# Kernel optimization log

Measured on AMD Instinct MI355X. Metric: run time of the kernel, lower is better.

Reference implementation:

```python
import jax, jax.numpy as jnp
import numpy as np

ECNUM = 100
CA1NUM = 100
CA3NUM = 100
ACTNUM = 2
TRACKLEN = 100
SIGMA = 5.0
BS = 4096


def setup_inputs() -> dict:
    key = jax.random.key(0)
    ks = jax.random.split(key, 10)
    cue_train = jax.random.randint(ks[0], (BS, TRACKLEN), 0, 3).astype(jnp.int32) - 1  # values in {-1,0,1}
    ec3_last = jax.random.uniform(ks[1], (BS, ECNUM), dtype=jnp.float32)
    ec5_last = jax.random.uniform(ks[2], (BS, ECNUM), dtype=jnp.float32)
    ca1_last = jnp.zeros((BS, CA1NUM), dtype=jnp.float32)
    cueL = (jax.random.uniform(ks[3], (ECNUM,)) < 0.2).astype(jnp.float32)
    cueR = (jax.random.uniform(ks[4], (ECNUM,)) < 0.2).astype(jnp.float32)
    Wec3ca1 = 0.01 * jax.random.uniform(ks[5], (ECNUM, CA1NUM), dtype=jnp.float32)
    Wca3ca1 = 0.01 * jax.random.uniform(ks[6], (CA3NUM, CA1NUM), dtype=jnp.float32)
    Wca1ec5 = 0.01 * jax.random.normal(ks[7], (CA1NUM, ECNUM), dtype=jnp.float32)
    Wca1act = 0.01 * jax.random.uniform(ks[8], (CA1NUM, ACTNUM), dtype=jnp.float32)
    ca1bias = 0.01 * jax.random.uniform(ks[9], (CA1NUM,), dtype=jnp.float32)
    return {
        "bs": BS,
        "cue_train": cue_train,
        "ec3_last": ec3_last,
        "ec5_last": ec5_last,
        "ca1_last": ca1_last,
        "cueL": cueL,
        "cueR": cueR,
        "Wec3ca1": Wec3ca1,
        "Wca3ca1": Wca3ca1,
        "Wca1ec5": Wca1ec5,
        "Wca1act": Wca1act,
        "ca1bias": ca1bias,
    }


def reference(bs, cue_train, ec3_last, ec5_last, ca1_last, cueL, cueR,
              Wec3ca1, Wca3ca1, Wca1ec5, Wca1act, ca1bias):
    # Precompute position-dependent CA3 activity for every timestep: [T, ca3num]
    centers = jnp.linspace(0.0, float(TRACKLEN), CA3NUM)
    xs = jnp.arange(TRACKLEN, dtype=jnp.float32)
    ca3_all = jnp.exp(-(((xs[:, None] - centers[None, :]) / SIGMA) ** 2) / 2.0)
    drive = ca3_all @ Wca3ca1  # [T, ca1num]

    # Sensory input per timestep via conditional gather: [T, bs, ecnum]
    cue_t = cue_train.T[:, :, None]  # [T, bs, 1]
    sensory = jnp.where(cue_t == 1, cueL[None, None, :],
                        jnp.where(cue_t == -1, cueR[None, None, :], 0.0))

    def step(carry, inp):
        ec3, ec5 = carry
        d, s = inp  # d: [ca1num], s: [bs, ecnum]
        ca1 = jax.nn.relu(d[None, :] * (1.0 + jax.nn.sigmoid(ec3 @ Wec3ca1)) - ca1bias)
        ec5 = ec5 + ca1 @ Wca1ec5
        ec5 = 0.69 + 0.3 * jax.nn.sigmoid(4.0 * (ec5 - 0.3))
        ec3 = ec5 * ec3 + s
        return (ec3, ec5), ca1

    (ec3, ec5), ca1his = jax.lax.scan(step, (ec3_last, ec5_last), (drive, sensory))
    ca1 = ca1his[-1]
    actCell = ca1 @ Wca1act
    return actCell, ca1his, ec3, ec5, ca1
```

## Files before the change

kernel.cpp:

```cpp
#include <hip/hip_runtime.h>

#define TLEN 100
#define ECN  100
#define CA1N 100
#define CA3N 100
#define BSZ  4096
#define ACTN 2
#define BT   16

typedef short bf16x8 __attribute__((ext_vector_type(8)));
typedef float f32x4  __attribute__((ext_vector_type(4)));

__device__ __forceinline__ unsigned short f2bf(float f){
  union { float f; unsigned int u; } c; c.f = f;
  return (unsigned short)((c.u + 0x8000u) >> 16);
}
__device__ __forceinline__ float fsigm(float x){
  float e = __expf(-x);
  return __builtin_amdgcn_rcpf(1.0f + e);
}

#define BAR_LGKM() asm volatile("s_waitcnt lgkmcnt(0)\n\ts_barrier" ::: "memory")

__global__ void drive_kernel(const float* __restrict__ Wca3ca1, float* __restrict__ drive){
  __shared__ float ca3row[CA3N];
  const int t = blockIdx.x, tid = threadIdx.x;
  if (tid < CA3N){
    float c = (float)tid * (100.0f / 99.0f);
    float d = ((float)t - c) * 0.2f;
    ca3row[tid] = __expf(-0.5f * d * d);
  }
  __syncthreads();
  if (tid < CA1N){
    float acc = 0.f;
    for (int k = 0; k < CA3N; ++k) acc = fmaf(ca3row[k], Wca3ca1[k*CA1N + tid], acc);
    drive[t*CA1N + tid] = acc;
  }
}


__global__ __launch_bounds__(512, 2)
void rnn_kernel(const int*   __restrict__ cue_train,
                const float* __restrict__ ec3_last,
                const float* __restrict__ ec5_last,
                const float* __restrict__ cueL,
                const float* __restrict__ cueR,
                const float* __restrict__ Wec3ca1,
                const float* __restrict__ Wca1ec5,
                const float* __restrict__ Wca1act,
                const float* __restrict__ ca1bias,
                const float* __restrict__ drive,
                float*       __restrict__ out)
{
  __shared__ __align__(16) unsigned short ec3b[4 * 64 * 8];
  __shared__ __align__(16) unsigned short ca1b[4 * 64 * 8];
  __shared__ __align__(16) float ca1f[BT * 132];
  __shared__ signed char cueT[TLEN * BT];

  const int tid = threadIdx.x;
  const int b0  = blockIdx.x * BT;

  float* out_act = out;
  float* out_his = out + (size_t)BSZ * ACTN;
  float* out_e3  = out_his + (size_t)TLEN * BSZ * CA1N;
  float* out_e5  = out_e3 + (size_t)BSZ * ECN;
  float* out_c1  = out_e5 + (size_t)BSZ * ECN;

  for (int idx = tid; idx < 4 * 64 * 8; idx += 512){ ec3b[idx] = 0; ca1b[idx] = 0; }
  for (int idx = tid; idx < BT * TLEN; idx += 512){
    int t = idx >> 4, r = idx & 15;
    cueT[idx] = (signed char)cue_train[(size_t)(b0 + r) * TLEN + t];
  }

  const int lane  = tid & 63;
  const int wv    = tid >> 6;
  const int col16 = lane & 15;
  const int q     = lane >> 4;
  const int col   = wv * 16 + col16;
  const bool okc  = (col < CA1N);
  const bool wactive = (wv < 7);
  const int colc  = okc ? col : 0;

  const int abase = (col >> 5) * 512 + ((col >> 3) & 3) * 128 + (col & 7) + q * 32;

  bf16x8 b1[4], b2[4];
  #pragma unroll
  for (int ks = 0; ks < 4; ++ks){
    #pragma unroll
    for (int jj = 0; jj < 8; ++jj){
      int k = ks * 32 + q * 8 + jj;
      float w1 = 0.f, w2 = 0.f;
      if (k < ECN && okc){
        w1 = Wec3ca1[k * CA1N + col];
        w2 = Wca1ec5[k * ECN  + col];
      }
      b1[ks][jj] = (short)f2bf(w1);
      b2[ks][jj] = (short)f2bf(w2);
    }
  }
  const float bias_c = okc ? ca1bias[col] : 0.f;
  const float cL = okc ? cueL[col] : 0.f;
  const float cR = okc ? cueR[col] : 0.f;

  __syncthreads();

  float ec3v[4], ec5v[4], c1[4] = {0.f,0.f,0.f,0.f};
  #pragma unroll
  for (int i = 0; i < 4; ++i){
    int r = q * 4 + i;
    float v3 = okc ? ec3_last[(size_t)(b0 + r) * ECN + col] : 0.f;
    float v5 = okc ? ec5_last[(size_t)(b0 + r) * ECN + col] : 0.f;
    ec3v[i] = v3; ec5v[i] = v5;
    if (okc) ec3b[abase + i * 8] = f2bf(v3);
  }
  __syncthreads();

  const float* dp = drive + colc;
  float* hp = out_his + (size_t)(b0 + q * 4) * CA1N + colc;

  const bf16x8* fe3 = (const bf16x8*)ec3b;
  const bf16x8* fc1 = (const bf16x8*)ca1b;

  float dv = *dp;

  for (int t = 0; t < TLEN; ++t){
    int cu4 = *(const int*)(cueT + t * BT + q * 4);

    if (wactive){
      f32x4 aA = {0.f,0.f,0.f,0.f}, aB = {0.f,0.f,0.f,0.f};
      bf16x8 a0 = fe3[  0 + lane];
      bf16x8 a1 = fe3[ 64 + lane];
      bf16x8 a2 = fe3[128 + lane];
      bf16x8 a3 = fe3[192 + lane];
      aA = __builtin_amdgcn_mfma_f32_16x16x32_bf16(a0, b1[0], aA, 0, 0, 0);
      aB = __builtin_amdgcn_mfma_f32_16x16x32_bf16(a1, b1[1], aB, 0, 0, 0);
      aA = __builtin_amdgcn_mfma_f32_16x16x32_bf16(a2, b1[2], aA, 0, 0, 0);
      aB = __builtin_amdgcn_mfma_f32_16x16x32_bf16(a3, b1[3], aB, 0, 0, 0);
      f32x4 z = aA + aB;
      float dmb = dv - bias_c;
      #pragma unroll
      for (int i = 0; i < 4; ++i){
        float v = fmaxf(fmaf(dv, fsigm(z[i]), dmb), 0.f);
        c1[i] = v;
        if (okc) ca1b[abase + i * 8] = f2bf(v);
      }
    }
    BAR_LGKM();

    if (okc){
      hp[0 * CA1N] = c1[0];
      hp[1 * CA1N] = c1[1];
      hp[2 * CA1N] = c1[2];
      hp[3 * CA1N] = c1[3];
    }
    hp += (size_t)BSZ * CA1N;

    dp += CA1N;
    float dv_next = (t + 1 < TLEN) ? *dp : 0.f;

    if (wactive){
      f32x4 aA = {0.f,0.f,0.f,0.f}, aB = {0.f,0.f,0.f,0.f};
      bf16x8 a0 = fc1[  0 + lane];
      bf16x8 a1 = fc1[ 64 + lane];
      bf16x8 a2 = fc1[128 + lane];
      bf16x8 a3 = fc1[192 + lane];
      aA = __builtin_amdgcn_mfma_f32_16x16x32_bf16(a0, b2[0], aA, 0, 0, 0);
      aB = __builtin_amdgcn_mfma_f32_16x16x32_bf16(a1, b2[1], aB, 0, 0, 0);
      aA = __builtin_amdgcn_mfma_f32_16x16x32_bf16(a2, b2[2], aA, 0, 0, 0);
      aB = __builtin_amdgcn_mfma_f32_16x16x32_bf16(a3, b2[3], aB, 0, 0, 0);
      f32x4 z2 = aA + aB;
      #pragma unroll
      for (int i = 0; i < 4; ++i){
        float x  = ec5v[i] + z2[i];
        float e5 = fmaf(0.3f, fsigm(fmaf(4.0f, x, -1.2f)), 0.69f);
        ec5v[i] = e5;
        int cu = (cu4 >> (8 * i)) & 0xff;
        float sns = (cu == 1) ? cL : ((cu == 0xff) ? cR : 0.0f);
        float e3 = fmaf(e5, ec3v[i], sns);
        ec3v[i] = e3;
        if (okc) ec3b[abase + i * 8] = f2bf(e3);
      }
    }
    BAR_LGKM();
    dv = dv_next;
  }

  if (okc){
    #pragma unroll
    for (int i = 0; i < 4; ++i){
      int r = q * 4 + i;
      size_t g = (size_t)(b0 + r) * ECN + col;
      out_e3[g] = ec3v[i];
      out_e5[g] = ec5v[i];
      out_c1[g] = c1[i];
      ca1f[r * 132 + col] = c1[i];
    }
  }
  __syncthreads();

  if (tid < BT * ACTN){
    int r = tid >> 1, a = tid & 1;
    float acc = 0.f;
    for (int jj = 0; jj < CA1N; ++jj)
      acc = fmaf(ca1f[r * 132 + jj], Wca1act[jj * ACTN + a], acc);
    out_act[(size_t)(b0 + r) * ACTN + a] = acc;
  }
}

extern "C" void kernel_launch(void* const* d_in, const int* in_sizes, int n_in,
                              void* d_out, int out_size, void* d_ws, size_t ws_size,
                              hipStream_t stream) {
  (void)in_sizes; (void)n_in; (void)out_size; (void)ws_size;
  const int*   cue_train = (const int*)  d_in[1];
  const float* ec3_last  = (const float*)d_in[2];
  const float* ec5_last  = (const float*)d_in[3];
  const float* cueL      = (const float*)d_in[5];
  const float* cueR      = (const float*)d_in[6];
  const float* Wec3ca1   = (const float*)d_in[7];
  const float* Wca3ca1   = (const float*)d_in[8];
  const float* Wca1ec5   = (const float*)d_in[9];
  const float* Wca1act   = (const float*)d_in[10];
  const float* ca1bias   = (const float*)d_in[11];
  float* out   = (float*)d_out;
  float* drive = (float*)d_ws;

  drive_kernel<<<TLEN, 128, 0, stream>>>(Wca3ca1, drive);
  rnn_kernel<<<BSZ / BT, 512, 0, stream>>>(cue_train, ec3_last, ec5_last,
                                           cueL, cueR, Wec3ca1, Wca1ec5,
                                           Wca1act, ca1bias, drive, out);
}
```

Measured before the change: 270.1 us.

## Halve block to 4 waves, each computing two 16-column MFMA tiles

Shrinks the RNN block from 8 to 4 wavefronts, with each wave now owning two 16-column output tiles. The A fragments loaded from LDS are reused across both tiles, and the per-step barriers synchronise fewer waves. In exchange each wave does twice the serial work on the critical path and keeps twice as many weight fragments in registers. Occupancy also changes under the new launch bounds.

```diff
diff --git a/kernel.cpp b/kernel.cpp
--- a/kernel.cpp
+++ b/kernel.cpp
@@ -39,7 +39,7 @@
 }
 
 
-__global__ __launch_bounds__(512, 2)
+__global__ __launch_bounds__(256, 1)
 void rnn_kernel(const int*   __restrict__ cue_train,
                 const float* __restrict__ ec3_last,
                 const float* __restrict__ ec5_last,
@@ -66,8 +66,8 @@
   float* out_e5  = out_e3 + (size_t)BSZ * ECN;
   float* out_c1  = out_e5 + (size_t)BSZ * ECN;
 
-  for (int idx = tid; idx < 4 * 64 * 8; idx += 512){ ec3b[idx] = 0; ca1b[idx] = 0; }
-  for (int idx = tid; idx < BT * TLEN; idx += 512){
+  for (int idx = tid; idx < 4 * 64 * 8; idx += 256){ ec3b[idx] = 0; ca1b[idx] = 0; }
+  for (int idx = tid; idx < BT * TLEN; idx += 256){
     int t = idx >> 4, r = idx & 15;
     cueT[idx] = (signed char)cue_train[(size_t)(b0 + r) * TLEN + t];
   }
@@ -76,124 +76,189 @@
   const int wv    = tid >> 6;
   const int col16 = lane & 15;
   const int q     = lane >> 4;
-  const int col   = wv * 16 + col16;
-  const bool okc  = (col < CA1N);
-  const bool wactive = (wv < 7);
-  const int colc  = okc ? col : 0;
-
-  const int abase = (col >> 5) * 512 + ((col >> 3) & 3) * 128 + (col & 7) + q * 32;
-
-  bf16x8 b1[4], b2[4];
+  const int tl0   = wv * 2;
+  const int tl1   = wv * 2 + 1;
+  const int col0  = tl0 * 16 + col16;
+  const int col1  = tl1 * 16 + col16;
+  const bool ok0  = (col0 < CA1N);
+  const bool ok1  = (col1 < CA1N);
+  const bool live1 = (tl1 < 7);
+  const int col0c = ok0 ? col0 : 0;
+  const int col1c = ok1 ? col1 : 0;
+
+  const int ab0 = (col0 >> 5) * 512 + ((col0 >> 3) & 3) * 128 + (col0 & 7) + q * 32;
+  const int ab1 = (col1 >> 5) * 512 + ((col1 >> 3) & 3) * 128 + (col1 & 7) + q * 32;
+
+  bf16x8 b1[2][4], b2[2][4];
   #pragma unroll
   for (int ks = 0; ks < 4; ++ks){
     #pragma unroll
     for (int jj = 0; jj < 8; ++jj){
       int k = ks * 32 + q * 8 + jj;
-      float w1 = 0.f, w2 = 0.f;
-      if (k < ECN && okc){
-        w1 = Wec3ca1[k * CA1N + col];
-        w2 = Wca1ec5[k * ECN  + col];
-      }
-      b1[ks][jj] = (short)f2bf(w1);
-      b2[ks][jj] = (short)f2bf(w2);
-    }
-  }
-  const float bias_c = okc ? ca1bias[col] : 0.f;
-  const float cL = okc ? cueL[col] : 0.f;
-  const float cR = okc ? cueR[col] : 0.f;
-
-  __syncthreads();
-
-  float ec3v[4], ec5v[4], c1[4] = {0.f,0.f,0.f,0.f};
+      float w10 = 0.f, w20 = 0.f, w11 = 0.f, w21 = 0.f;
+      if (k < ECN){
+        if (ok0){ w10 = Wec3ca1[k * CA1N + col0]; w20 = Wca1ec5[k * ECN + col0]; }
+        if (ok1){ w11 = Wec3ca1[k * CA1N + col1]; w21 = Wca1ec5[k * ECN + col1]; }
+      }
+      b1[0][ks][jj] = (short)f2bf(w10);
+      b2[0][ks][jj] = (short)f2bf(w20);
+      b1[1][ks][jj] = (short)f2bf(w11);
+      b2[1][ks][jj] = (short)f2bf(w21);
+    }
+  }
+  const float bias0 = ok0 ? ca1bias[col0] : 0.f;
+  const float bias1 = ok1 ? ca1bias[col1] : 0.f;
+  const float cL0 = ok0 ? cueL[col0] : 0.f;
+  const float cR0 = ok0 ? cueR[col0] : 0.f;
+  const float cL1 = ok1 ? cueL[col1] : 0.f;
+  const float cR1 = ok1 ? cueR[col1] : 0.f;
+
+  __syncthreads();
+
+  float ec3v[2][4], ec5v[2][4], c1[2][4];
   #pragma unroll
   for (int i = 0; i < 4; ++i){
     int r = q * 4 + i;
-    float v3 = okc ? ec3_last[(size_t)(b0 + r) * ECN + col] : 0.f;
-    float v5 = okc ? ec5_last[(size_t)(b0 + r) * ECN + col] : 0.f;
-    ec3v[i] = v3; ec5v[i] = v5;
-    if (okc) ec3b[abase + i * 8] = f2bf(v3);
-  }
-  __syncthreads();
-
-  const float* dp = drive + colc;
-  float* hp = out_his + (size_t)(b0 + q * 4) * CA1N + colc;
+    float v30 = ok0 ? ec3_last[(size_t)(b0 + r) * ECN + col0] : 0.f;
+    float v50 = ok0 ? ec5_last[(size_t)(b0 + r) * ECN + col0] : 0.f;
+    float v31 = ok1 ? ec3_last[(size_t)(b0 + r) * ECN + col1] : 0.f;
+    float v51 = ok1 ? ec5_last[(size_t)(b0 + r) * ECN + col1] : 0.f;
+    ec3v[0][i] = v30; ec5v[0][i] = v50; c1[0][i] = 0.f;
+    ec3v[1][i] = v31; ec5v[1][i] = v51; c1[1][i] = 0.f;
+    if (ok0) ec3b[ab0 + i * 8] = f2bf(v30);
+    if (ok1) ec3b[ab1 + i * 8] = f2bf(v31);
+  }
+  __syncthreads();
+
+  const float* dp = drive + CA1N;
+  float dv0 = drive[col0c];
+  float dv1 = drive[col1c];
+  float* hp0 = out_his + (size_t)(b0 + q * 4) * CA1N + col0c;
+  float* hp1 = out_his + (size_t)(b0 + q * 4) * CA1N + col1c;
 
   const bf16x8* fe3 = (const bf16x8*)ec3b;
   const bf16x8* fc1 = (const bf16x8*)ca1b;
 
-  float dv = *dp;
-
   for (int t = 0; t < TLEN; ++t){
     int cu4 = *(const int*)(cueT + t * BT + q * 4);
 
-    if (wactive){
-      f32x4 aA = {0.f,0.f,0.f,0.f}, aB = {0.f,0.f,0.f,0.f};
+    {
       bf16x8 a0 = fe3[  0 + lane];
       bf16x8 a1 = fe3[ 64 + lane];
       bf16x8 a2 = fe3[128 + lane];
       bf16x8 a3 = fe3[192 + lane];
-      aA = __builtin_amdgcn_mfma_f32_16x16x32_bf16(a0, b1[0], aA, 0, 0, 0);
-      aB = __builtin_amdgcn_mfma_f32_16x16x32_bf16(a1, b1[1], aB, 0, 0, 0);
-      aA = __builtin_amdgcn_mfma_f32_16x16x32_bf16(a2, b1[2], aA, 0, 0, 0);
-      aB = __builtin_amdgcn_mfma_f32_16x16x32_bf16(a3, b1[3], aB, 0, 0, 0);
-      f32x4 z = aA + aB;
-      float dmb = dv - bias_c;
+      f32x4 aA = {0.f,0.f,0.f,0.f}, aB = {0.f,0.f,0.f,0.f};
+      aA = __builtin_amdgcn_mfma_f32_16x16x32_bf16(a0, b1[0][0], aA, 0, 0, 0);
+      aB = __builtin_amdgcn_mfma_f32_16x16x32_bf16(a1, b1[0][1], aB, 0, 0, 0);
+      aA = __builtin_amdgcn_mfma_f32_16x16x32_bf16(a2, b1[0][2], aA, 0, 0, 0);
+      aB = __builtin_amdgcn_mfma_f32_16x16x32_bf16(a3, b1[0][3], aB, 0, 0, 0);
+      f32x4 z0 = aA + aB;
+      float dmb0 = dv0 - bias0;
       #pragma unroll
       for (int i = 0; i < 4; ++i){
-        float v = fmaxf(fmaf(dv, fsigm(z[i]), dmb), 0.f);
-        c1[i] = v;
-        if (okc) ca1b[abase + i * 8] = f2bf(v);
+        float v = fmaxf(fmaf(dv0, fsigm(z0[i]), dmb0), 0.f);
+        c1[0][i] = v;
+        if (ok0) ca1b[ab0 + i * 8] = f2bf(v);
+      }
+      if (live1){
+        f32x4 cA = {0.f,0.f,0.f,0.f}, cB = {0.f,0.f,0.f,0.f};
+        cA = __builtin_amdgcn_mfma_f32_16x16x32_bf16(a0, b1[1][0], cA, 0, 0, 0);
+        cB = __builtin_amdgcn_mfma_f32_16x16x32_bf16(a1, b1[1][1], cB, 0, 0, 0);
+        cA = __builtin_amdgcn_mfma_f32_16x16x32_bf16(a2, b1[1][2], cA, 0, 0, 0);
+        cB = __builtin_amdgcn_mfma_f32_16x16x32_bf16(a3, b1[1][3], cB, 0, 0, 0);
+        f32x4 z1 = cA + cB;
+        float dmb1 = dv1 - bias1;
+        #pragma unroll
+        for (int i = 0; i < 4; ++i){
+          float v = fmaxf(fmaf(dv1, fsigm(z1[i]), dmb1), 0.f);
+          c1[1][i] = v;
+          if (ok1) ca1b[ab1 + i * 8] = f2bf(v);
+        }
       }
     }
     BAR_LGKM();
 
-    if (okc){
-      hp[0 * CA1N] = c1[0];
-      hp[1 * CA1N] = c1[1];
-      hp[2 * CA1N] = c1[2];
-      hp[3 * CA1N] = c1[3];
-    }
-    hp += (size_t)BSZ * CA1N;
-
+    if (ok0){
+      hp0[0 * CA1N] = c1[0][0];
+      hp0[1 * CA1N] = c1[0][1];
+      hp0[2 * CA1N] = c1[0][2];
+      hp0[3 * CA1N] = c1[0][3];
+    }
+    if (live1 && ok1){
+      hp1[0 * CA1N] = c1[1][0];
+      hp1[1 * CA1N] = c1[1][1];
+      hp1[2 * CA1N] = c1[1][2];
+      hp1[3 * CA1N] = c1[1][3];
+    }
+    hp0 += (size_t)BSZ * CA1N;
+    hp1 += (size_t)BSZ * CA1N;
+
+    float nv0 = 0.f, nv1 = 0.f;
+    if (t + 1 < TLEN){ nv0 = dp[col0c]; nv1 = dp[col1c]; }
     dp += CA1N;
-    float dv_next = (t + 1 < TLEN) ? *dp : 0.f;
-
-    if (wactive){
-      f32x4 aA = {0.f,0.f,0.f,0.f}, aB = {0.f,0.f,0.f,0.f};
+
+    {
       bf16x8 a0 = fc1[  0 + lane];
       bf16x8 a1 = fc1[ 64 + lane];
       bf16x8 a2 = fc1[128 + lane];
       bf16x8 a3 = fc1[192 + lane];
-      aA = __builtin_amdgcn_mfma_f32_16x16x32_bf16(a0, b2[0], aA, 0, 0, 0);
-      aB = __builtin_amdgcn_mfma_f32_16x16x32_bf16(a1, b2[1], aB, 0, 0, 0);
-      aA = __builtin_amdgcn_mfma_f32_16x16x32_bf16(a2, b2[2], aA, 0, 0, 0);
-      aB = __builtin_amdgcn_mfma_f32_16x16x32_bf16(a3, b2[3], aB, 0, 0, 0);
+      f32x4 aA = {0.f,0.f,0.f,0.f}, aB = {0.f,0.f,0.f,0.f};
+      aA = __builtin_amdgcn_mfma_f32_16x16x32_bf16(a0, b2[0][0], aA, 0, 0, 0);
+      aB = __builtin_amdgcn_mfma_f32_16x16x32_bf16(a1, b2[0][1], aB, 0, 0, 0);
+      aA = __builtin_amdgcn_mfma_f32_16x16x32_bf16(a2, b2[0][2], aA, 0, 0, 0);
+      aB = __builtin_amdgcn_mfma_f32_16x16x32_bf16(a3, b2[0][3], aB, 0, 0, 0);
       f32x4 z2 = aA + aB;
       #pragma unroll
       for (int i = 0; i < 4; ++i){
-        float x  = ec5v[i] + z2[i];
+        float x  = ec5v[0][i] + z2[i];
         float e5 = fmaf(0.3f, fsigm(fmaf(4.0f, x, -1.2f)), 0.69f);
-        ec5v[i] = e5;
+        ec5v[0][i] = e5;
         int cu = (cu4 >> (8 * i)) & 0xff;
-        float sns = (cu == 1) ? cL : ((cu == 0xff) ? cR : 0.0f);
-        float e3 = fmaf(e5, ec3v[i], sns);
-        ec3v[i] = e3;
-        if (okc) ec3b[abase + i * 8] = f2bf(e3);
+        float sns = (cu == 1) ? cL0 : ((cu == 0xff) ? cR0 : 0.0f);
+        float e3 = fmaf(e5, ec3v[0][i], sns);
+        ec3v[0][i] = e3;
+        if (ok0) ec3b[ab0 + i * 8] = f2bf(e3);
+      }
+      if (live1){
+        f32x4 cA = {0.f,0.f,0.f,0.f}, cB = {0.f,0.f,0.f,0.f};
+        cA = __builtin_amdgcn_mfma_f32_16x16x32_bf16(a0, b2[1][0], cA, 0, 0, 0);
+        cB = __builtin_amdgcn_mfma_f32_16x16x32_bf16(a1, b2[1][1], cB, 0, 0, 0);
+        cA = __builtin_amdgcn_mfma_f32_16x16x32_bf16(a2, b2[1][2], cA, 0, 0, 0);
+        cB = __builtin_amdgcn_mfma_f32_16x16x32_bf16(a3, b2[1][3], cB, 0, 0, 0);
+        f32x4 z21 = cA + cB;
+        #pragma unroll
+        for (int i = 0; i < 4; ++i){
+          float x  = ec5v[1][i] + z21[i];
+          float e5 = fmaf(0.3f, fsigm(fmaf(4.0f, x, -1.2f)), 0.69f);
+          ec5v[1][i] = e5;
+          int cu = (cu4 >> (8 * i)) & 0xff;
+          float sns = (cu == 1) ? cL1 : ((cu == 0xff) ? cR1 : 0.0f);
+          float e3 = fmaf(e5, ec3v[1][i], sns);
+          ec3v[1][i] = e3;
+          if (ok1) ec3b[ab1 + i * 8] = f2bf(e3);
+        }
       }
     }
     BAR_LGKM();
-    dv = dv_next;
-  }
-
-  if (okc){
-    #pragma unroll
-    for (int i = 0; i < 4; ++i){
-      int r = q * 4 + i;
-      size_t g = (size_t)(b0 + r) * ECN + col;
-      out_e3[g] = ec3v[i];
-      out_e5[g] = ec5v[i];
-      out_c1[g] = c1[i];
-      ca1f[r * 132 + col] = c1[i];
+    dv0 = nv0; dv1 = nv1;
+  }
+
+  #pragma unroll
+  for (int i = 0; i < 4; ++i){
+    int r = q * 4 + i;
+    if (ok0){
+      size_t g = (size_t)(b0 + r) * ECN + col0;
+      out_e3[g] = ec3v[0][i];
+      out_e5[g] = ec5v[0][i];
+      out_c1[g] = c1[0][i];
+      ca1f[r * 132 + col0] = c1[0][i];
+    }
+    if (live1 && ok1){
+      size_t g = (size_t)(b0 + r) * ECN + col1;
+      out_e3[g] = ec3v[1][i];
+      out_e5[g] = ec5v[1][i];
+      out_c1[g] = c1[1][i];
+      ca1f[r * 132 + col1] = c1[1][i];
     }
   }
   __syncthreads();
@@ -225,7 +290,7 @@
   float* drive = (float*)d_ws;
 
   drive_kernel<<<TLEN, 128, 0, stream>>>(Wca3ca1, drive);
-  rnn_kernel<<<BSZ / BT, 512, 0, stream>>>(cue_train, ec3_last, ec5_last,
+  rnn_kernel<<<BSZ / BT, 256, 0, stream>>>(cue_train, ec3_last, ec5_last,
                                            cueL, cueR, Wec3ca1, Wca1ec5,
                                            Wca1act, ca1bias, drive, out);
 }
```

Result: slower. 291.2 us (+7.8%).

## Interleave two batch groups per block to overlap their dependent recurrence stages

Applied to the files above, without the earlier changes.

Each block now handles 32 batch rows as two 16-row groups run half a step out of phase. In each barrier phase, one group's CA1 stage and the other group's EC5/EC3 stage run back to back, so their MFMAs and sigmoids are independent and can interleave. This is meant to hide MFMA latency and halve the barriers per row. The price is twice the register state per thread and half as many blocks (128), which lowers GPU-wide occupancy. There is also a skewed prologue and epilogue to handle the phase offset.

```diff
diff --git a/kernel.cpp b/kernel.cpp
--- a/kernel.cpp
+++ b/kernel.cpp
@@ -6,7 +6,7 @@
 #define CA3N 100
 #define BSZ  4096
 #define ACTN 2
-#define BT   16
+#define BT   32
 
 typedef short bf16x8 __attribute__((ext_vector_type(8)));
 typedef float f32x4  __attribute__((ext_vector_type(4)));
@@ -52,8 +52,8 @@
                 const float* __restrict__ drive,
                 float*       __restrict__ out)
 {
-  __shared__ __align__(16) unsigned short ec3b[4 * 64 * 8];
-  __shared__ __align__(16) unsigned short ca1b[4 * 64 * 8];
+  __shared__ __align__(16) unsigned short ec3b[2 * 2048];
+  __shared__ __align__(16) unsigned short ca1b[2 * 2048];
   __shared__ __align__(16) float ca1f[BT * 132];
   __shared__ signed char cueT[TLEN * BT];
 
@@ -66,9 +66,9 @@
   float* out_e5  = out_e3 + (size_t)BSZ * ECN;
   float* out_c1  = out_e5 + (size_t)BSZ * ECN;
 
-  for (int idx = tid; idx < 4 * 64 * 8; idx += 512){ ec3b[idx] = 0; ca1b[idx] = 0; }
+  for (int idx = tid; idx < 2 * 2048; idx += 512){ ec3b[idx] = 0; ca1b[idx] = 0; }
   for (int idx = tid; idx < BT * TLEN; idx += 512){
-    int t = idx >> 4, r = idx & 15;
+    int t = idx >> 5, r = idx & 31;
     cueT[idx] = (signed char)cue_train[(size_t)(b0 + r) * TLEN + t];
   }
 
@@ -104,96 +104,168 @@
 
   __syncthreads();
 
-  float ec3v[4], ec5v[4], c1[4] = {0.f,0.f,0.f,0.f};
+  float e3v0[4], e5v0[4], c10[4] = {0.f,0.f,0.f,0.f};
+  float e3v1[4], e5v1[4], c11[4] = {0.f,0.f,0.f,0.f};
   #pragma unroll
   for (int i = 0; i < 4; ++i){
-    int r = q * 4 + i;
-    float v3 = okc ? ec3_last[(size_t)(b0 + r) * ECN + col] : 0.f;
-    float v5 = okc ? ec5_last[(size_t)(b0 + r) * ECN + col] : 0.f;
-    ec3v[i] = v3; ec5v[i] = v5;
-    if (okc) ec3b[abase + i * 8] = f2bf(v3);
+    int r0 = q * 4 + i, r1 = 16 + q * 4 + i;
+    float a3 = okc ? ec3_last[(size_t)(b0 + r0) * ECN + col] : 0.f;
+    float a5 = okc ? ec5_last[(size_t)(b0 + r0) * ECN + col] : 0.f;
+    float g3 = okc ? ec3_last[(size_t)(b0 + r1) * ECN + col] : 0.f;
+    float g5 = okc ? ec5_last[(size_t)(b0 + r1) * ECN + col] : 0.f;
+    e3v0[i] = a3; e5v0[i] = a5; e3v1[i] = g3; e5v1[i] = g5;
+    if (okc){
+      ec3b[abase + i * 8]        = f2bf(a3);
+      ec3b[2048 + abase + i * 8] = f2bf(g3);
+    }
   }
   __syncthreads();
 
+  const bf16x8* fe30 = (const bf16x8*)ec3b;
+  const bf16x8* fe31 = (const bf16x8*)(ec3b + 2048);
+  const bf16x8* fc10 = (const bf16x8*)ca1b;
+  const bf16x8* fc11 = (const bf16x8*)(ca1b + 2048);
+
   const float* dp = drive + colc;
-  float* hp = out_his + (size_t)(b0 + q * 4) * CA1N + colc;
-
-  const bf16x8* fe3 = (const bf16x8*)ec3b;
-  const bf16x8* fc1 = (const bf16x8*)ca1b;
-
-  float dv = *dp;
+  float dva = dp[0];
+  float dvb = dp[CA1N];
+  dp += 2 * CA1N;
+
+  float* hp0 = out_his + (size_t)(b0 + q * 4) * CA1N + colc;
+  float* hp1 = out_his + (size_t)(b0 + 16 + q * 4) * CA1N + colc;
+
+  if (wactive){
+    bf16x8 a0 = fe30[  0 + lane], a1 = fe30[ 64 + lane];
+    bf16x8 a2 = fe30[128 + lane], a3 = fe30[192 + lane];
+    f32x4 aA = {0.f,0.f,0.f,0.f}, aB = {0.f,0.f,0.f,0.f};
+    aA = __builtin_amdgcn_mfma_f32_16x16x32_bf16(a0, b1[0], aA, 0, 0, 0);
+    aB = __builtin_amdgcn_mfma_f32_16x16x32_bf16(a1, b1[1], aB, 0, 0, 0);
+    aA = __builtin_amdgcn_mfma_f32_16x16x32_bf16(a2, b1[2], aA, 0, 0, 0);
+    aB = __builtin_amdgcn_mfma_f32_16x16x32_bf16(a3, b1[3], aB, 0, 0, 0);
+    f32x4 z = aA + aB;
+    float dmb = dva - bias_c;
+    #pragma unroll
+    for (int i = 0; i < 4; ++i){
+      float v = fmaxf(fmaf(dva, fsigm(z[i]), dmb), 0.f);
+      c10[i] = v;
+      if (okc) ca1b[abase + i * 8] = f2bf(v);
+    }
+    if (okc){
+      hp0[0 * CA1N] = c10[0]; hp0[1 * CA1N] = c10[1];
+      hp0[2 * CA1N] = c10[2]; hp0[3 * CA1N] = c10[3];
+    }
+  }
+  hp0 += (size_t)BSZ * CA1N;
+  BAR_LGKM();
 
   for (int t = 0; t < TLEN; ++t){
-    int cu4 = *(const int*)(cueT + t * BT + q * 4);
+    int cu40 = *(const int*)(cueT + t * BT + q * 4);
+    int cu41 = *(const int*)(cueT + t * BT + 16 + q * 4);
 
     if (wactive){
-      f32x4 aA = {0.f,0.f,0.f,0.f}, aB = {0.f,0.f,0.f,0.f};
-      bf16x8 a0 = fe3[  0 + lane];
-      bf16x8 a1 = fe3[ 64 + lane];
-      bf16x8 a2 = fe3[128 + lane];
-      bf16x8 a3 = fe3[192 + lane];
-      aA = __builtin_amdgcn_mfma_f32_16x16x32_bf16(a0, b1[0], aA, 0, 0, 0);
-      aB = __builtin_amdgcn_mfma_f32_16x16x32_bf16(a1, b1[1], aB, 0, 0, 0);
-      aA = __builtin_amdgcn_mfma_f32_16x16x32_bf16(a2, b1[2], aA, 0, 0, 0);
-      aB = __builtin_amdgcn_mfma_f32_16x16x32_bf16(a3, b1[3], aB, 0, 0, 0);
-      f32x4 z = aA + aB;
-      float dmb = dv - bias_c;
+      bf16x8 e0 = fe31[  0 + lane], e1 = fe31[ 64 + lane];
+      bf16x8 e2 = fe31[128 + lane], e3 = fe31[192 + lane];
+      bf16x8 u0 = fc10[  0 + lane], u1 = fc10[ 64 + lane];
+      bf16x8 u2 = fc10[128 + lane], u3 = fc10[192 + lane];
+      f32x4 pA = {0.f,0.f,0.f,0.f}, pB = {0.f,0.f,0.f,0.f};
+      f32x4 rA = {0.f,0.f,0.f,0.f}, rB = {0.f,0.f,0.f,0.f};
+      pA = __builtin_amdgcn_mfma_f32_16x16x32_bf16(e0, b1[0], pA, 0, 0, 0);
+      rA = __builtin_amdgcn_mfma_f32_16x16x32_bf16(u0, b2[0], rA, 0, 0, 0);
+      pB = __builtin_amdgcn_mfma_f32_16x16x32_bf16(e1, b1[1], pB, 0, 0, 0);
+      rB = __builtin_amdgcn_mfma_f32_16x16x32_bf16(u1, b2[1], rB, 0, 0, 0);
+      pA = __builtin_amdgcn_mfma_f32_16x16x32_bf16(e2, b1[2], pA, 0, 0, 0);
+      rA = __builtin_amdgcn_mfma_f32_16x16x32_bf16(u2, b2[2], rA, 0, 0, 0);
+      pB = __builtin_amdgcn_mfma_f32_16x16x32_bf16(e3, b1[3], pB, 0, 0, 0);
+      rB = __builtin_amdgcn_mfma_f32_16x16x32_bf16(u3, b2[3], rB, 0, 0, 0);
+      f32x4 z1 = pA + pB;
+      f32x4 z20 = rA + rB;
+      float dmb = dva - bias_c;
       #pragma unroll
       for (int i = 0; i < 4; ++i){
-        float v = fmaxf(fmaf(dv, fsigm(z[i]), dmb), 0.f);
-        c1[i] = v;
-        if (okc) ca1b[abase + i * 8] = f2bf(v);
-      }
-    }
-    BAR_LGKM();
-
-    if (okc){
-      hp[0 * CA1N] = c1[0];
-      hp[1 * CA1N] = c1[1];
-      hp[2 * CA1N] = c1[2];
-      hp[3 * CA1N] = c1[3];
-    }
-    hp += (size_t)BSZ * CA1N;
-
-    dp += CA1N;
-    float dv_next = (t + 1 < TLEN) ? *dp : 0.f;
-
-    if (wactive){
-      f32x4 aA = {0.f,0.f,0.f,0.f}, aB = {0.f,0.f,0.f,0.f};
-      bf16x8 a0 = fc1[  0 + lane];
-      bf16x8 a1 = fc1[ 64 + lane];
-      bf16x8 a2 = fc1[128 + lane];
-      bf16x8 a3 = fc1[192 + lane];
-      aA = __builtin_amdgcn_mfma_f32_16x16x32_bf16(a0, b2[0], aA, 0, 0, 0);
-      aB = __builtin_amdgcn_mfma_f32_16x16x32_bf16(a1, b2[1], aB, 0, 0, 0);
-      aA = __builtin_amdgcn_mfma_f32_16x16x32_bf16(a2, b2[2], aA, 0, 0, 0);
-      aB = __builtin_amdgcn_mfma_f32_16x16x32_bf16(a3, b2[3], aB, 0, 0, 0);
-      f32x4 z2 = aA + aB;
+        float v = fmaxf(fmaf(dva, fsigm(z1[i]), dmb), 0.f);
+        c11[i] = v;
+        if (okc) ca1b[2048 + abase + i * 8] = f2bf(v);
+      }
       #pragma unroll
       for (int i = 0; i < 4; ++i){
-        float x  = ec5v[i] + z2[i];
+        float x  = e5v0[i] + z20[i];
         float e5 = fmaf(0.3f, fsigm(fmaf(4.0f, x, -1.2f)), 0.69f);
-        ec5v[i] = e5;
-        int cu = (cu4 >> (8 * i)) & 0xff;
+        e5v0[i] = e5;
+        int cu = (cu40 >> (8 * i)) & 0xff;
         float sns = (cu == 1) ? cL : ((cu == 0xff) ? cR : 0.0f);
-        float e3 = fmaf(e5, ec3v[i], sns);
-        ec3v[i] = e3;
-        if (okc) ec3b[abase + i * 8] = f2bf(e3);
-      }
-    }
+        float e3n = fmaf(e5, e3v0[i], sns);
+        e3v0[i] = e3n;
+        if (okc) ec3b[abase + i * 8] = f2bf(e3n);
+      }
+      if (okc){
+        hp1[0 * CA1N] = c11[0]; hp1[1 * CA1N] = c11[1];
+        hp1[2 * CA1N] = c11[2]; hp1[3 * CA1N] = c11[3];
+      }
+    }
+    hp1 += (size_t)BSZ * CA1N;
     BAR_LGKM();
-    dv = dv_next;
+
+    float dnx = (t + 2 < TLEN) ? dp[0] : 0.f;
+    dp += CA1N;
+    const bool doG0 = (t + 1 < TLEN);
+
+    if (wactive){
+      bf16x8 e0 = fe30[  0 + lane], e1 = fe30[ 64 + lane];
+      bf16x8 e2 = fe30[128 + lane], e3 = fe30[192 + lane];
+      bf16x8 u0 = fc11[  0 + lane], u1 = fc11[ 64 + lane];
+      bf16x8 u2 = fc11[128 + lane], u3 = fc11[192 + lane];
+      f32x4 pA = {0.f,0.f,0.f,0.f}, pB = {0.f,0.f,0.f,0.f};
+      f32x4 rA = {0.f,0.f,0.f,0.f}, rB = {0.f,0.f,0.f,0.f};
+      pA = __builtin_amdgcn_mfma_f32_16x16x32_bf16(e0, b1[0], pA, 0, 0, 0);
+      rA = __builtin_amdgcn_mfma_f32_16x16x32_bf16(u0, b2[0], rA, 0, 0, 0);
+      pB = __builtin_amdgcn_mfma_f32_16x16x32_bf16(e1, b1[1], pB, 0, 0, 0);
+      rB = __builtin_amdgcn_mfma_f32_16x16x32_bf16(u1, b2[1], rB, 0, 0, 0);
+      pA = __builtin_amdgcn_mfma_f32_16x16x32_bf16(e2, b1[2], pA, 0, 0, 0);
+      rA = __builtin_amdgcn_mfma_f32_16x16x32_bf16(u2, b2[2], rA, 0, 0, 0);
+      pB = __builtin_amdgcn_mfma_f32_16x16x32_bf16(e3, b1[3], pB, 0, 0, 0);
+      rB = __builtin_amdgcn_mfma_f32_16x16x32_bf16(u3, b2[3], rB, 0, 0, 0);
+      f32x4 z0 = pA + pB;
+      f32x4 z21 = rA + rB;
+      #pragma unroll
+      for (int i = 0; i < 4; ++i){
+        float x  = e5v1[i] + z21[i];
+        float e5 = fmaf(0.3f, fsigm(fmaf(4.0f, x, -1.2f)), 0.69f);
+        e5v1[i] = e5;
+        int cu = (cu41 >> (8 * i)) & 0xff;
+        float sns = (cu == 1) ? cL : ((cu == 0xff) ? cR : 0.0f);
+        float e3n = fmaf(e5, e3v1[i], sns);
+        e3v1[i] = e3n;
+        if (okc) ec3b[2048 + abase + i * 8] = f2bf(e3n);
+      }
+      if (doG0){
+        float dmb = dvb - bias_c;
+        #pragma unroll
+        for (int i = 0; i < 4; ++i){
+          float v = fmaxf(fmaf(dvb, fsigm(z0[i]), dmb), 0.f);
+          c10[i] = v;
+          if (okc) ca1b[abase + i * 8] = f2bf(v);
+        }
+        if (okc){
+          hp0[0 * CA1N] = c10[0]; hp0[1 * CA1N] = c10[1];
+          hp0[2 * CA1N] = c10[2]; hp0[3 * CA1N] = c10[3];
+        }
+      }
+    }
+    hp0 += (size_t)BSZ * CA1N;
+    BAR_LGKM();
+    dva = dvb; dvb = dnx;
   }
 
   if (okc){
     #pragma unroll
     for (int i = 0; i < 4; ++i){
-      int r = q * 4 + i;
-      size_t g = (size_t)(b0 + r) * ECN + col;
-      out_e3[g] = ec3v[i];
-      out_e5[g] = ec5v[i];
-      out_c1[g] = c1[i];
-      ca1f[r * 132 + col] = c1[i];
+      int r0 = q * 4 + i, r1 = 16 + q * 4 + i;
+      size_t g0 = (size_t)(b0 + r0) * ECN + col;
+      size_t g1 = (size_t)(b0 + r1) * ECN + col;
+      out_e3[g0] = e3v0[i]; out_e5[g0] = e5v0[i]; out_c1[g0] = c10[i];
+      out_e3[g1] = e3v1[i]; out_e5[g1] = e5v1[i]; out_c1[g1] = c11[i];
+      ca1f[r0 * 132 + col] = c10[i];
+      ca1f[r1 * 132 + col] = c11[i];
     }
   }
   __syncthreads();
```

After: 310.8 us. 15.1% more time.
